# Kernel tuning notes

Measured on AMD Instinct MI355X. Metric: run time of the kernel, lower is better.

Reference implementation:

```python
import jax, jax.numpy as jnp
import numpy as np

NUM_HEADS = 8
DIM = 256  # == out_dim; module implicitly requires dim == out_dim


def setup_inputs() -> dict:
    key = jax.random.key(0)
    k0, k1, k2, k3, k4, k5 = jax.random.split(key, 6)
    B, N, T, dim = 4, 128, 128, DIM
    s = dim ** -0.5
    return {
        "v": jax.random.normal(k0, (B, N, T, dim), dtype=jnp.float32),
        "Wq": jax.random.normal(k1, (dim, dim), dtype=jnp.float32) * s,
        "Wk": jax.random.normal(k2, (dim, dim), dtype=jnp.float32) * s,
        "Wv": jax.random.normal(k3, (dim, dim), dtype=jnp.float32) * s,
        "Wp": jax.random.normal(k4, (dim, dim), dtype=jnp.float32) * s,
        "bp": jax.random.normal(k5, (dim,), dtype=jnp.float32) * 0.01,
    }


def reference(v, Wq, Wk, Wv, Wp, bp):
    B, N, T, dim = v.shape
    H = NUM_HEADS
    hd = dim // H
    scale = hd ** -0.5
    # projections (qkv_bias=False)
    q = (v @ Wq).reshape(B * N, T, H, hd)
    k = (v @ Wk).reshape(B * N, T, H, hd)
    vv = (v @ Wv).reshape(B * N, T, H, hd)
    # NOTE: heads axis is NOT moved before the matmul in the original torch
    # code, so attention is over the HEADS axis: per (b*n, t) an HxH matrix.
    attn = jnp.einsum('mthd,mtgd->mthg', q, k) * scale  # [B*N, T, H, H]
    attn = jax.nn.softmax(attn, axis=-1)
    x = jnp.einsum('mthg,mtgd->mthd', attn, vv).reshape(B, N, T, dim)
    # output projection (with bias); dropout probs are 0 / eval mode
    return x @ Wp + bp
```

## Files before the change

### kernel.cpp

```cpp
#include <hip/hip_runtime.h>
#include <hip/hip_bf16.h>
#include <math.h>


#define DIMX      256
#define NH        8
#define HD        32
#define TM        32
#define NTHREADS  512
#define QSTRIDE   776
#define KT        8
#define NT_QKV    48

typedef _Float16 f16x8 __attribute__((ext_vector_type(8)));
typedef _Float16 f16x4 __attribute__((ext_vector_type(4)));
typedef _Float16 f16x2 __attribute__((ext_vector_type(2)));
typedef float    f32x4 __attribute__((ext_vector_type(4)));

static __device__ __forceinline__ f16x2 pkrtz(float a, float b) {
    return (f16x2)__builtin_amdgcn_cvt_pkrtz(a, b);
}

__global__ void pack_weights(const float* __restrict__ Wq,
                             const float* __restrict__ Wk,
                             const float* __restrict__ Wv,
                             const float* __restrict__ Wp,
                             _Float16* __restrict__ pk)
{
    const int QKV_FRAGS = NT_QKV * KT * 64;
    int u = blockIdx.x * blockDim.x + threadIdx.x;
    const float* W;
    int nt, kt, lane;
    if (u < QKV_FRAGS) {
        nt = u / (KT * 64); kt = (u / 64) % KT; lane = u % 64;
        if (nt < 16)      { W = Wq; }
        else if (nt < 32) { W = Wk; nt -= 16; }
        else              { W = Wv; nt -= 32; }
    } else {
        int u2 = u - QKV_FRAGS;
        nt = u2 / (KT * 64); kt = (u2 / 64) % KT; lane = u2 % 64;
        W = Wp;
    }
    const int n  = nt * 16 + (lane & 15);
    const int k0 = kt * 32 + (lane >> 4) * 8;
    f16x8 frag;
#pragma unroll
    for (int j = 0; j < 8; ++j)
        frag[j] = (_Float16)W[(size_t)(k0 + j) * DIMX + n];
    *(f16x8*)(pk + (size_t)u * 8) = frag;
}

__global__ __launch_bounds__(NTHREADS, 6)
void fused_attn_mfma(const float* __restrict__ v,
                     const _Float16* __restrict__ Wqkv_pk,
                     const _Float16* __restrict__ Wp_pk,
                     const float* __restrict__ bp,
                     float* __restrict__ out)
{
    __shared__ __align__(16) _Float16 S[TM * QSTRIDE];

    const int tid   = threadIdx.x;
    const int lane  = tid & 63;
    const int wv_id = tid >> 6;
    const int l15   = lane & 15;
    const int quad  = lane >> 4;
    const long token0 = (long)blockIdx.x * TM;

    {
        const float4* src = (const float4*)(v + token0 * DIMX);
#pragma unroll
        for (int i = 0; i < 4; ++i) {
            int u = tid + NTHREADS * i;
            int m = u >> 6;
            int c = (u & 63) * 4;
            float4 t4 = src[u];
            f16x2 lo = pkrtz(t4.x, t4.y), hi = pkrtz(t4.z, t4.w);
            f16x4 b4 = { lo.x, lo.y, hi.x, hi.y };
            *(f16x4*)&S[m * QSTRIDE + c] = b4;
        }
    }
    __syncthreads();

    f32x4 acc1[2][3];
    int tiles1[3] = { 2 * wv_id, 2 * wv_id + 1, 40 + wv_id };
    {
        int tiles0[3] = { 16 + wv_id * 3, 17 + wv_id * 3, 18 + wv_id * 3 };

        f32x4 acc0[2][3];
#pragma unroll
        for (int tt = 0; tt < 2; ++tt)
#pragma unroll
            for (int j = 0; j < 3; ++j)
                acc0[tt][j] = (f32x4){0.f, 0.f, 0.f, 0.f};
        {
            const f16x8* wb = (const f16x8*)Wqkv_pk + lane;
            f16x8 wcur[3];
#pragma unroll
            for (int j = 0; j < 3; ++j)
                wcur[j] = wb[(size_t)(tiles0[j] * KT) * 64];
            for (int kt = 0; kt < KT; ++kt) {
                const int ktn = (kt + 1 < KT) ? kt + 1 : KT - 1;
                f16x8 wnxt[3];
#pragma unroll
                for (int j = 0; j < 3; ++j)
                    wnxt[j] = wb[(size_t)(tiles0[j] * KT + ktn) * 64];
                f16x8 vf[2];
#pragma unroll
                for (int tt = 0; tt < 2; ++tt)
                    vf[tt] = *(const f16x8*)&S[(tt * 16 + l15) * QSTRIDE + kt * 32 + quad * 8];
#pragma unroll
                for (int j = 0; j < 3; ++j) {
                    acc0[0][j] = __builtin_amdgcn_mfma_f32_16x16x32_f16(wcur[j], vf[0], acc0[0][j], 0, 0, 0);
                    acc0[1][j] = __builtin_amdgcn_mfma_f32_16x16x32_f16(wcur[j], vf[1], acc0[1][j], 0, 0, 0);
                }
#pragma unroll
                for (int j = 0; j < 3; ++j) wcur[j] = wnxt[j];
            }
        }
#pragma unroll
        for (int tt = 0; tt < 2; ++tt)
#pragma unroll
            for (int j = 0; j < 3; ++j) {
                f16x2 a = pkrtz(acc0[tt][j][0], acc0[tt][j][1]);
                f16x2 b = pkrtz(acc0[tt][j][2], acc0[tt][j][3]);
                f16x4 p4 = { a.x, a.y, b.x, b.y };
                *(f16x4*)&S[(tt * 16 + l15) * QSTRIDE + tiles0[j] * 16 + quad * 4] = p4;
            }

#pragma unroll
        for (int tt = 0; tt < 2; ++tt)
#pragma unroll
            for (int j = 0; j < 3; ++j)
                acc1[tt][j] = (f32x4){0.f, 0.f, 0.f, 0.f};
        {
            const f16x8* wb = (const f16x8*)Wqkv_pk + lane;
            f16x8 wcur[3];
#pragma unroll
            for (int j = 0; j < 3; ++j)
                wcur[j] = wb[(size_t)(tiles1[j] * KT) * 64];
            for (int kt = 0; kt < KT; ++kt) {
                const int ktn = (kt + 1 < KT) ? kt + 1 : KT - 1;
                f16x8 wnxt[3];
#pragma unroll
                for (int j = 0; j < 3; ++j)
                    wnxt[j] = wb[(size_t)(tiles1[j] * KT + ktn) * 64];
                f16x8 vf[2];
#pragma unroll
                for (int tt = 0; tt < 2; ++tt)
                    vf[tt] = *(const f16x8*)&S[(tt * 16 + l15) * QSTRIDE + kt * 32 + quad * 8];
#pragma unroll
                for (int j = 0; j < 3; ++j) {
                    acc1[0][j] = __builtin_amdgcn_mfma_f32_16x16x32_f16(wcur[j], vf[0], acc1[0][j], 0, 0, 0);
                    acc1[1][j] = __builtin_amdgcn_mfma_f32_16x16x32_f16(wcur[j], vf[1], acc1[1][j], 0, 0, 0);
                }
#pragma unroll
                for (int j = 0; j < 3; ++j) wcur[j] = wnxt[j];
            }
        }
    }
    __syncthreads();

#pragma unroll
    for (int tt = 0; tt < 2; ++tt)
#pragma unroll
        for (int j = 0; j < 3; ++j) {
            f16x2 a = pkrtz(acc1[tt][j][0], acc1[tt][j][1]);
            f16x2 b = pkrtz(acc1[tt][j][2], acc1[tt][j][3]);
            f16x4 p4 = { a.x, a.y, b.x, b.y };
            *(f16x4*)&S[(tt * 16 + l15) * QSTRIDE + tiles1[j] * 16 + quad * 4] = p4;
        }
    __syncthreads();

    {
        const int ta  = tid >> 4;
        const int sub = tid & 15;
        const int h   = sub >> 1;
        const int d0  = (sub & 1) * 16;
        const float scale = 0.17677669529663687f;

        const _Float16* qrow  = &S[ta * QSTRIDE + h * HD + d0];
        const _Float16* kbase = &S[ta * QSTRIDE + 256 + d0];
        const _Float16* vbase = &S[ta * QSTRIDE + 512 + d0];

        f16x8 q0 = *(const f16x8*)qrow;
        f16x8 q1 = *(const f16x8*)(qrow + 8);

        float logits[NH];
#pragma unroll
        for (int g = 0; g < NH; ++g) {
            f16x8 k0 = *(const f16x8*)(kbase + g * HD);
            f16x8 k1 = *(const f16x8*)(kbase + g * HD + 8);
            f16x8 p  = q0 * k0;
            p += q1 * k1;
            f16x4 r4 = __builtin_shufflevector(p, p, 0, 1, 2, 3)
                     + __builtin_shufflevector(p, p, 4, 5, 6, 7);
            f16x2 r2 = __builtin_shufflevector(r4, r4, 0, 1)
                     + __builtin_shufflevector(r4, r4, 2, 3);
            logits[g] = (float)r2.x + (float)r2.y;
        }
#pragma unroll
        for (int g = 0; g < NH; ++g)
            logits[g] = (logits[g] + __shfl_xor(logits[g], 1, 64)) * scale;

        float mx = logits[0];
#pragma unroll
        for (int g = 1; g < NH; ++g) mx = fmaxf(mx, logits[g]);
        float se = 0.f;
#pragma unroll
        for (int g = 0; g < NH; ++g) { logits[g] = __expf(logits[g] - mx); se += logits[g]; }
        float inv = 1.f / se;

        f16x8 xa0 = (f16x8)(_Float16)0.f;
        f16x8 xa1 = (f16x8)(_Float16)0.f;
#pragma unroll
        for (int g = 0; g < NH; ++g) {
            _Float16 ph = (_Float16)(logits[g] * inv);
            f16x8 pw = { ph, ph, ph, ph, ph, ph, ph, ph };
            f16x8 v0 = *(const f16x8*)(vbase + g * HD);
            f16x8 v1 = *(const f16x8*)(vbase + g * HD + 8);
            xa0 += pw * v0;
            xa1 += pw * v1;
        }
        __syncthreads();
        *(f16x8*)&S[ta * QSTRIDE + h * HD + d0]     = xa0;
        *(f16x8*)&S[ta * QSTRIDE + h * HD + d0 + 8] = xa1;
    }
    __syncthreads();

    {
        const int nt0 = wv_id * 2;
        f32x4 acc[2][2];
#pragma unroll
        for (int tt = 0; tt < 2; ++tt)
#pragma unroll
            for (int j = 0; j < 2; ++j)
                acc[tt][j] = (f32x4){0.f, 0.f, 0.f, 0.f};

        const f16x8* wb = (const f16x8*)Wp_pk + lane;
        f16x8 wcur[2];
#pragma unroll
        for (int j = 0; j < 2; ++j)
            wcur[j] = wb[(size_t)((nt0 + j) * KT) * 64];

        for (int kt = 0; kt < KT; ++kt) {
            const int ktn = (kt + 1 < KT) ? kt + 1 : KT - 1;
            f16x8 wnxt[2];
#pragma unroll
            for (int j = 0; j < 2; ++j)
                wnxt[j] = wb[(size_t)((nt0 + j) * KT + ktn) * 64];
            f16x8 xf[2];
#pragma unroll
            for (int tt = 0; tt < 2; ++tt)
                xf[tt] = *(const f16x8*)&S[(tt * 16 + l15) * QSTRIDE + kt * 32 + quad * 8];
#pragma unroll
            for (int j = 0; j < 2; ++j) {
                acc[0][j] = __builtin_amdgcn_mfma_f32_16x16x32_f16(wcur[j], xf[0], acc[0][j], 0, 0, 0);
                acc[1][j] = __builtin_amdgcn_mfma_f32_16x16x32_f16(wcur[j], xf[1], acc[1][j], 0, 0, 0);
            }
#pragma unroll
            for (int j = 0; j < 2; ++j) wcur[j] = wnxt[j];
        }
#pragma unroll
        for (int j = 0; j < 2; ++j) {
            f32x4 b = *(const f32x4*)&bp[(nt0 + j) * 16 + quad * 4];
#pragma unroll
            for (int tt = 0; tt < 2; ++tt) {
                f32x4 o = acc[tt][j] + b;
                *(f32x4*)&out[(token0 + tt * 16 + l15) * DIMX + (nt0 + j) * 16 + quad * 4] = o;
            }
        }
    }
}

extern "C" void kernel_launch(void* const* d_in, const int* in_sizes, int n_in,
                              void* d_out, int out_size, void* d_ws, size_t ws_size,
                              hipStream_t stream) {
    const float* v  = (const float*)d_in[0];
    const float* Wq = (const float*)d_in[1];
    const float* Wk = (const float*)d_in[2];
    const float* Wv = (const float*)d_in[3];
    const float* Wp = (const float*)d_in[4];
    const float* bp = (const float*)d_in[5];
    float* out = (float*)d_out;

    _Float16* pk = (_Float16*)d_ws;
    const _Float16* Wqkv_pk = pk;
    const _Float16* Wp_pk   = pk + (size_t)24576 * 8;

    pack_weights<<<256, 128, 0, stream>>>(Wq, Wk, Wv, Wp, pk);

    const int ntokens = in_sizes[0] / DIMX;
    fused_attn_mfma<<<ntokens / TM, NTHREADS, 0, stream>>>(v, Wqkv_pk, Wp_pk, bp, out);
}
```

Before: 158.7 us.

## Double token tile per block with separate V buffer and 1024 threads

Each block now processes 64 tokens with 16 waves. The input now lives in its own padded LDS region, so all 48 QKV output tiles are computed in one pass without the earlier two-phase overwrite and its extra barrier. Each weight fragment fetched from global memory is reused across four token sub-tiles instead of two, and weight prefetch runs two k-steps ahead. LDS use per block grows to about 133 KB and the block size doubles, which may reduce blocks per CU and latency hiding.

Measured after the change: 163.9 us. 1.03x slower.

```diff
diff --git a/kernel.cpp b/kernel.cpp
--- a/kernel.cpp
+++ b/kernel.cpp
@@ -1,16 +1,18 @@
 #include <hip/hip_runtime.h>
-#include <hip/hip_bf16.h>
 #include <math.h>
 
 
 #define DIMX      256
 #define NH        8
 #define HD        32
-#define TM        32
-#define NTHREADS  512
+#define TM        64
+#define NTHREADS  1024
+#define VSTRIDE   264
 #define QSTRIDE   776
 #define KT        8
 #define NT_QKV    48
+#define NJ1       3
+#define TT        4
 
 typedef _Float16 f16x8 __attribute__((ext_vector_type(8)));
 typedef _Float16 f16x4 __attribute__((ext_vector_type(4)));
@@ -50,14 +52,16 @@
     *(f16x8*)(pk + (size_t)u * 8) = frag;
 }
 
-__global__ __launch_bounds__(NTHREADS, 6)
+__global__ __launch_bounds__(NTHREADS, 4)
 void fused_attn_mfma(const float* __restrict__ v,
                      const _Float16* __restrict__ Wqkv_pk,
                      const _Float16* __restrict__ Wp_pk,
                      const float* __restrict__ bp,
                      float* __restrict__ out)
 {
-    __shared__ __align__(16) _Float16 S[TM * QSTRIDE];
+    __shared__ __align__(16) _Float16 S[TM * VSTRIDE + TM * QSTRIDE];
+    _Float16* V   = S;
+    _Float16* QKV = S + TM * VSTRIDE;
 
     const int tid   = threadIdx.x;
     const int lane  = tid & 63;
@@ -76,99 +80,58 @@
             float4 t4 = src[u];
             f16x2 lo = pkrtz(t4.x, t4.y), hi = pkrtz(t4.z, t4.w);
             f16x4 b4 = { lo.x, lo.y, hi.x, hi.y };
-            *(f16x4*)&S[m * QSTRIDE + c] = b4;
+            *(f16x4*)&V[m * VSTRIDE + c] = b4;
         }
     }
     __syncthreads();
 
-    f32x4 acc1[2][3];
-    int tiles1[3] = { 2 * wv_id, 2 * wv_id + 1, 40 + wv_id };
-    {
-        int tiles0[3] = { 16 + wv_id * 3, 17 + wv_id * 3, 18 + wv_id * 3 };
-
-        f32x4 acc0[2][3];
-#pragma unroll
-        for (int tt = 0; tt < 2; ++tt)
-#pragma unroll
-            for (int j = 0; j < 3; ++j)
-                acc0[tt][j] = (f32x4){0.f, 0.f, 0.f, 0.f};
-        {
-            const f16x8* wb = (const f16x8*)Wqkv_pk + lane;
-            f16x8 wcur[3];
-#pragma unroll
-            for (int j = 0; j < 3; ++j)
-                wcur[j] = wb[(size_t)(tiles0[j] * KT) * 64];
-            for (int kt = 0; kt < KT; ++kt) {
-                const int ktn = (kt + 1 < KT) ? kt + 1 : KT - 1;
-                f16x8 wnxt[3];
-#pragma unroll
-                for (int j = 0; j < 3; ++j)
-                    wnxt[j] = wb[(size_t)(tiles0[j] * KT + ktn) * 64];
-                f16x8 vf[2];
-#pragma unroll
-                for (int tt = 0; tt < 2; ++tt)
-                    vf[tt] = *(const f16x8*)&S[(tt * 16 + l15) * QSTRIDE + kt * 32 + quad * 8];
-#pragma unroll
-                for (int j = 0; j < 3; ++j) {
-                    acc0[0][j] = __builtin_amdgcn_mfma_f32_16x16x32_f16(wcur[j], vf[0], acc0[0][j], 0, 0, 0);
-                    acc0[1][j] = __builtin_amdgcn_mfma_f32_16x16x32_f16(wcur[j], vf[1], acc0[1][j], 0, 0, 0);
-                }
-#pragma unroll
-                for (int j = 0; j < 3; ++j) wcur[j] = wnxt[j];
+    {
+        const int t0 = wv_id * NJ1;
+        f32x4 acc[TT][NJ1];
+#pragma unroll
+        for (int tt = 0; tt < TT; ++tt)
+#pragma unroll
+            for (int j = 0; j < NJ1; ++j)
+                acc[tt][j] = (f32x4){0.f, 0.f, 0.f, 0.f};
+
+        const f16x8* wb = (const f16x8*)Wqkv_pk + lane;
+        f16x8 w0[NJ1], w1[NJ1];
+#pragma unroll
+        for (int j = 0; j < NJ1; ++j) {
+            w0[j] = wb[(size_t)((t0 + j) * KT + 0) * 64];
+            w1[j] = wb[(size_t)((t0 + j) * KT + 1) * 64];
+        }
+        for (int kt = 0; kt < KT; ++kt) {
+            const int ktp = (kt + 2 < KT) ? kt + 2 : KT - 1;
+            f16x8 wn[NJ1];
+#pragma unroll
+            for (int j = 0; j < NJ1; ++j)
+                wn[j] = wb[(size_t)((t0 + j) * KT + ktp) * 64];
+
+            f16x8 vf[TT];
+#pragma unroll
+            for (int tt = 0; tt < TT; ++tt)
+                vf[tt] = *(const f16x8*)&V[(tt * 16 + l15) * VSTRIDE + kt * 32 + quad * 8];
+
+#pragma unroll
+            for (int j = 0; j < NJ1; ++j)
+#pragma unroll
+                for (int tt = 0; tt < TT; ++tt)
+                    acc[tt][j] = __builtin_amdgcn_mfma_f32_16x16x32_f16(w0[j], vf[tt], acc[tt][j], 0, 0, 0);
+
+#pragma unroll
+            for (int j = 0; j < NJ1; ++j) { w0[j] = w1[j]; w1[j] = wn[j]; }
+        }
+#pragma unroll
+        for (int tt = 0; tt < TT; ++tt)
+#pragma unroll
+            for (int j = 0; j < NJ1; ++j) {
+                f16x2 a = pkrtz(acc[tt][j][0], acc[tt][j][1]);
+                f16x2 b = pkrtz(acc[tt][j][2], acc[tt][j][3]);
+                f16x4 p4 = { a.x, a.y, b.x, b.y };
+                *(f16x4*)&QKV[(tt * 16 + l15) * QSTRIDE + (t0 + j) * 16 + quad * 4] = p4;
             }
-        }
-#pragma unroll
-        for (int tt = 0; tt < 2; ++tt)
-#pragma unroll
-            for (int j = 0; j < 3; ++j) {
-                f16x2 a = pkrtz(acc0[tt][j][0], acc0[tt][j][1]);
-                f16x2 b = pkrtz(acc0[tt][j][2], acc0[tt][j][3]);
-                f16x4 p4 = { a.x, a.y, b.x, b.y };
-                *(f16x4*)&S[(tt * 16 + l15) * QSTRIDE + tiles0[j] * 16 + quad * 4] = p4;
-            }
-
-#pragma unroll
-        for (int tt = 0; tt < 2; ++tt)
-#pragma unroll
-            for (int j = 0; j < 3; ++j)
-                acc1[tt][j] = (f32x4){0.f, 0.f, 0.f, 0.f};
-        {
-            const f16x8* wb = (const f16x8*)Wqkv_pk + lane;
-            f16x8 wcur[3];
-#pragma unroll
-            for (int j = 0; j < 3; ++j)
-                wcur[j] = wb[(size_t)(tiles1[j] * KT) * 64];
-            for (int kt = 0; kt < KT; ++kt) {
-                const int ktn = (kt + 1 < KT) ? kt + 1 : KT - 1;
-                f16x8 wnxt[3];
-#pragma unroll
-                for (int j = 0; j < 3; ++j)
-                    wnxt[j] = wb[(size_t)(tiles1[j] * KT + ktn) * 64];
-                f16x8 vf[2];
-#pragma unroll
-                for (int tt = 0; tt < 2; ++tt)
-                    vf[tt] = *(const f16x8*)&S[(tt * 16 + l15) * QSTRIDE + kt * 32 + quad * 8];
-#pragma unroll
-                for (int j = 0; j < 3; ++j) {
-                    acc1[0][j] = __builtin_amdgcn_mfma_f32_16x16x32_f16(wcur[j], vf[0], acc1[0][j], 0, 0, 0);
-                    acc1[1][j] = __builtin_amdgcn_mfma_f32_16x16x32_f16(wcur[j], vf[1], acc1[1][j], 0, 0, 0);
-                }
-#pragma unroll
-                for (int j = 0; j < 3; ++j) wcur[j] = wnxt[j];
-            }
-        }
-    }
-    __syncthreads();
-
-#pragma unroll
-    for (int tt = 0; tt < 2; ++tt)
-#pragma unroll
-        for (int j = 0; j < 3; ++j) {
-            f16x2 a = pkrtz(acc1[tt][j][0], acc1[tt][j][1]);
-            f16x2 b = pkrtz(acc1[tt][j][2], acc1[tt][j][3]);
-            f16x4 p4 = { a.x, a.y, b.x, b.y };
-            *(f16x4*)&S[(tt * 16 + l15) * QSTRIDE + tiles1[j] * 16 + quad * 4] = p4;
-        }
+    }
     __syncthreads();
 
     {
@@ -178,9 +141,9 @@
         const int d0  = (sub & 1) * 16;
         const float scale = 0.17677669529663687f;
 
-        const _Float16* qrow  = &S[ta * QSTRIDE + h * HD + d0];
-        const _Float16* kbase = &S[ta * QSTRIDE + 256 + d0];
-        const _Float16* vbase = &S[ta * QSTRIDE + 512 + d0];
+        const _Float16* qrow  = &QKV[ta * QSTRIDE + h * HD + d0];
+        const _Float16* kbase = &QKV[ta * QSTRIDE + 256 + d0];
+        const _Float16* vbase = &QKV[ta * QSTRIDE + 512 + d0];
 
         f16x8 q0 = *(const f16x8*)qrow;
         f16x8 q1 = *(const f16x8*)(qrow + 8);
@@ -221,53 +184,42 @@
             xa0 += pw * v0;
             xa1 += pw * v1;
         }
-        __syncthreads();
-        *(f16x8*)&S[ta * QSTRIDE + h * HD + d0]     = xa0;
-        *(f16x8*)&S[ta * QSTRIDE + h * HD + d0 + 8] = xa1;
+        *(f16x8*)&V[ta * VSTRIDE + h * HD + d0]     = xa0;
+        *(f16x8*)&V[ta * VSTRIDE + h * HD + d0 + 8] = xa1;
     }
     __syncthreads();
 
     {
-        const int nt0 = wv_id * 2;
-        f32x4 acc[2][2];
-#pragma unroll
-        for (int tt = 0; tt < 2; ++tt)
-#pragma unroll
-            for (int j = 0; j < 2; ++j)
-                acc[tt][j] = (f32x4){0.f, 0.f, 0.f, 0.f};
+        const int nt = wv_id;
+        f32x4 acc[TT];
+#pragma unroll
+        for (int tt = 0; tt < TT; ++tt)
+            acc[tt] = (f32x4){0.f, 0.f, 0.f, 0.f};
 
         const f16x8* wb = (const f16x8*)Wp_pk + lane;
-        f16x8 wcur[2];
-#pragma unroll
-        for (int j = 0; j < 2; ++j)
-            wcur[j] = wb[(size_t)((nt0 + j) * KT) * 64];
+        f16x8 w0 = wb[(size_t)(nt * KT + 0) * 64];
+        f16x8 w1 = wb[(size_t)(nt * KT + 1) * 64];
 
         for (int kt = 0; kt < KT; ++kt) {
-            const int ktn = (kt + 1 < KT) ? kt + 1 : KT - 1;
-            f16x8 wnxt[2];
-#pragma unroll
-            for (int j = 0; j < 2; ++j)
-                wnxt[j] = wb[(size_t)((nt0 + j) * KT + ktn) * 64];
-            f16x8 xf[2];
-#pragma unroll
-            for (int tt = 0; tt < 2; ++tt)
-                xf[tt] = *(const f16x8*)&S[(tt * 16 + l15) * QSTRIDE + kt * 32 + quad * 8];
-#pragma unroll
-            for (int j = 0; j < 2; ++j) {
-                acc[0][j] = __builtin_amdgcn_mfma_f32_16x16x32_f16(wcur[j], xf[0], acc[0][j], 0, 0, 0);
-                acc[1][j] = __builtin_amdgcn_mfma_f32_16x16x32_f16(wcur[j], xf[1], acc[1][j], 0, 0, 0);
-            }
-#pragma unroll
-            for (int j = 0; j < 2; ++j) wcur[j] = wnxt[j];
-        }
-#pragma unroll
-        for (int j = 0; j < 2; ++j) {
-            f32x4 b = *(const f32x4*)&bp[(nt0 + j) * 16 + quad * 4];
-#pragma unroll
-            for (int tt = 0; tt < 2; ++tt) {
-                f32x4 o = acc[tt][j] + b;
-                *(f32x4*)&out[(token0 + tt * 16 + l15) * DIMX + (nt0 + j) * 16 + quad * 4] = o;
-            }
+            const int ktp = (kt + 2 < KT) ? kt + 2 : KT - 1;
+            f16x8 wn = wb[(size_t)(nt * KT + ktp) * 64];
+
+            f16x8 xf[TT];
+#pragma unroll
+            for (int tt = 0; tt < TT; ++tt)
+                xf[tt] = *(const f16x8*)&V[(tt * 16 + l15) * VSTRIDE + kt * 32 + quad * 8];
+
+#pragma unroll
+            for (int tt = 0; tt < TT; ++tt)
+                acc[tt] = __builtin_amdgcn_mfma_f32_16x16x32_f16(w0, xf[tt], acc[tt], 0, 0, 0);
+
+            w0 = w1; w1 = wn;
+        }
+        f32x4 b = *(const f32x4*)&bp[nt * 16 + quad * 4];
+#pragma unroll
+        for (int tt = 0; tt < TT; ++tt) {
+            f32x4 o = acc[tt] + b;
+            *(f32x4*)&out[(token0 + tt * 16 + l15) * DIMX + nt * 16 + quad * 4] = o;
         }
     }
 }
```
